# Kernel tuning notes

Measured on AMD Instinct MI355X. Metric: run time of the kernel, lower is better.

The kernel has to match this reference:

```python
import jax, jax.numpy as jnp
import numpy as np
from jax import lax

F = 64          # nb_filters
K_DOWN = 4      # size_kernel_sample
K_RES = 3       # size_kernel_res
DIL = 3         # rate_dilation_res
N_DOWN = 3      # downsampling blocks (one level)
N_RES = 4       # residual sub-blocks per block
N_EMB = 512     # codebook size
BETA = 0.25


def conv1d(x, w, b, stride=1, dil=1, act=True):
    # x: (B,T,C), w: (K,Cin,Cout)
    y = lax.conv_general_dilated(x, w, (stride,), 'SAME', rhs_dilation=(dil,),
                                 dimension_numbers=('NWC', 'WIO', 'NWC')) + b
    return jax.nn.relu(y) if act else y


def conv1d_t(x, w, b, stride):
    # transposed conv, w: (K, Cin, Cout)
    y = lax.conv_transpose(x, w, (stride,), 'SAME',
                           dimension_numbers=('NWC', 'WIO', 'NWC')) + b
    return jax.nn.relu(y)


def setup_inputs() -> dict:
    key = jax.random.key(0)
    ks = jax.random.split(key, 12)
    s_in = 1.0 / np.sqrt(K_DOWN * 1)
    s_f = 1.0 / np.sqrt(K_DOWN * F)
    s_r = 1.0 / np.sqrt(K_RES * F)
    return {
        'x': jax.random.normal(ks[0], (4, 65536, 1), dtype=jnp.float32),
        'w_down0': jax.random.normal(ks[1], (K_DOWN, 1, F), dtype=jnp.float32) * s_in,
        'b_down0': jnp.zeros((F,), jnp.float32),
        'w_down': jax.random.normal(ks[2], (N_DOWN - 1, K_DOWN, F, F), dtype=jnp.float32) * s_f,
        'b_down': jnp.zeros((N_DOWN - 1, F), jnp.float32),
        'w_res_enc': jax.random.normal(ks[3], (N_DOWN, N_RES, 2, K_RES, F, F), dtype=jnp.float32) * s_r,
        'b_res_enc': jnp.zeros((N_DOWN, N_RES, 2, F), jnp.float32),
        'codebook': jax.random.normal(ks[4], (N_EMB, F), dtype=jnp.float32),
        'w_res_dec': jax.random.normal(ks[5], (N_DOWN, N_RES, 2, K_RES, F, F), dtype=jnp.float32) * s_r,
        'b_res_dec': jnp.zeros((N_DOWN, N_RES, 2, F), jnp.float32),
        'w_up': jax.random.normal(ks[6], (N_DOWN, K_DOWN, F, F), dtype=jnp.float32) * s_f,
        'b_up': jnp.zeros((N_DOWN, F), jnp.float32),
        'w_proj': jax.random.normal(ks[7], (K_RES, F, 1), dtype=jnp.float32) * s_r,
        'b_proj': jnp.zeros((1,), jnp.float32),
    }


def reference(x, w_down0, b_down0, w_down, b_down, w_res_enc, b_res_enc,
              codebook, w_res_dec, b_res_dec, w_up, b_up, w_proj, b_proj):
    # ---- Encoder: N_DOWN stride-2 downsampling blocks, each followed by
    # N_RES ForwardResidualSubBlocks (dilated conv -> conv, residual add) ----
    h = conv1d(x, w_down0, b_down0, stride=2)
    for blk in range(N_DOWN):
        if blk > 0:
            h = conv1d(h, w_down[blk - 1], b_down[blk - 1], stride=2)
        for r in range(N_RES):
            y = conv1d(h, w_res_enc[blk, r, 0], b_res_enc[blk, r, 0], dil=DIL)
            y = conv1d(y, w_res_enc[blk, r, 1], b_res_enc[blk, r, 1], dil=1)
            h = h + y
    z_e = h  # (B, T/8, F)

    # ---- VectorQuantiser over channel axis ----
    dot = jnp.einsum('btd,kd->btk', z_e, codebook)          # tensordot
    nz = jnp.sum(jnp.square(z_e), axis=-1, keepdims=True)   # (B,T,1)
    ne = jnp.sum(jnp.square(codebook), axis=-1)             # (K,)
    dist = -2.0 * dot + nz + ne                             # squared cdist
    ids = jnp.argmin(dist, axis=-1)                         # (B,T)
    z_q = codebook[ids]                                     # embedding_lookup
    loss_commit = jnp.mean(jnp.linalg.norm(lax.stop_gradient(z_e) - z_q, axis=-1))
    loss_codebook = jnp.mean(jnp.linalg.norm(z_e - lax.stop_gradient(z_q), axis=-1))
    loss_vq = loss_codebook + BETA * loss_commit
    similarity = dot / jnp.sqrt(nz) / jnp.sqrt(ne)

    # ---- Decoder: residual blocks then stride-2 transposed conv, x N_DOWN ----
    h = z_q
    for blk in range(N_DOWN):
        for r in range(N_RES):
            y = conv1d(h, w_res_dec[blk, r, 0], b_res_dec[blk, r, 0], dil=1)
            y = conv1d(y, w_res_dec[blk, r, 1], b_res_dec[blk, r, 1], dil=DIL)
            h = h + y
        h = conv1d_t(h, w_up[blk], b_up[blk], stride=2)
    x_hat = conv1d(h, w_proj, b_proj, act=False)  # linear projection
    return x_hat, loss_vq, ids, similarity
```

## Files before the change

kernel.cpp:

```cpp
#include <hip/hip_runtime.h>
#include <cstdint>


#define OFF_LOSS 262144
#define OFF_IDS  262145
#define OFF_SIM  294913

__global__ __launch_bounds__(256) void down0_kernel(
    const float* __restrict__ x, const float* __restrict__ w,
    const float* __restrict__ bias, float* __restrict__ y)
{
  int idx = blockIdx.x * 256 + threadIdx.x;
  int co = idx & 63;
  int r  = idx >> 6;
  int t  = r & 32767;
  int b  = r >> 15;
  const float* xb = x + (size_t)b * 65536;
  float acc = bias[co];
  #pragma unroll
  for (int k = 0; k < 4; ++k) {
    int gt = 2 * t - 1 + k;
    float xv = ((unsigned)gt < 65536u) ? xb[gt] : 0.f;
    acc += xv * w[k * 64 + co];
  }
  y[(size_t)idx] = fmaxf(acc, 0.f);
}

template <int DIL, bool HAS_RES>
__global__ __launch_bounds__(256, 4) void conv3_kernel(
    const float* __restrict__ x, const float* __restrict__ w,
    const float* __restrict__ bias, const float* res,
    float* y, int T)
{
  constexpr int TT = 128;
  constexpr int XT = TT + 2 * DIL;
  constexpr int XS = XT + 1;
  __shared__ float xs[64 * XS];
  const int tid  = threadIdx.x;
  const int lane = tid & 63;
  const int b    = blockIdx.z;
  const int t0   = blockIdx.x * TT;
  const int wv   = __builtin_amdgcn_readfirstlane(tid >> 6);
  const int co0  = __builtin_amdgcn_readfirstlane(blockIdx.y * 32 + wv * 8);

  const float* xb = x + (size_t)b * T * 64;
  for (int e = tid; e < 16 * XT; e += 256) {
    int tl = e >> 4, cq = (e & 15) * 4;
    int gt = t0 - DIL + tl;
    float4 v = make_float4(0.f, 0.f, 0.f, 0.f);
    if ((unsigned)gt < (unsigned)T) v = *(const float4*)&xb[(size_t)gt * 64 + cq];
    xs[(cq + 0) * XS + tl] = v.x;
    xs[(cq + 1) * XS + tl] = v.y;
    xs[(cq + 2) * XS + tl] = v.z;
    xs[(cq + 3) * XS + tl] = v.w;
  }
  __syncthreads();

  float acc0[8] = {}, acc1[8] = {};
  const float* wb = w + co0;
  #pragma unroll 2
  for (int ci = 0; ci < 64; ++ci) {
    const float* xr = xs + ci * XS + lane;
    float a0 = xr[0],  a1 = xr[DIL],      a2 = xr[2 * DIL];
    float b0 = xr[64], b1 = xr[64 + DIL], b2 = xr[64 + 2 * DIL];
    const float* w0 = wb + (0 * 64 + ci) * 64;
    const float* w1 = wb + (1 * 64 + ci) * 64;
    const float* w2 = wb + (2 * 64 + ci) * 64;
    #pragma unroll
    for (int j = 0; j < 8; ++j) {
      float c0 = w0[j], c1 = w1[j], c2 = w2[j];
      acc0[j] = fmaf(a0, c0, fmaf(a1, c1, fmaf(a2, c2, acc0[j])));
      acc1[j] = fmaf(b0, c0, fmaf(b1, c1, fmaf(b2, c2, acc1[j])));
    }
  }

  float bs[8];
  #pragma unroll
  for (int j = 0; j < 8; ++j) bs[j] = bias[co0 + j];
  size_t o0 = ((size_t)b * T + t0 + lane) * 64 + co0;
  size_t o1 = o0 + (size_t)64 * 64;
  float4 r0a, r0b, r1a, r1b;
  r0a.x = fmaxf(acc0[0] + bs[0], 0.f); r0a.y = fmaxf(acc0[1] + bs[1], 0.f);
  r0a.z = fmaxf(acc0[2] + bs[2], 0.f); r0a.w = fmaxf(acc0[3] + bs[3], 0.f);
  r0b.x = fmaxf(acc0[4] + bs[4], 0.f); r0b.y = fmaxf(acc0[5] + bs[5], 0.f);
  r0b.z = fmaxf(acc0[6] + bs[6], 0.f); r0b.w = fmaxf(acc0[7] + bs[7], 0.f);
  r1a.x = fmaxf(acc1[0] + bs[0], 0.f); r1a.y = fmaxf(acc1[1] + bs[1], 0.f);
  r1a.z = fmaxf(acc1[2] + bs[2], 0.f); r1a.w = fmaxf(acc1[3] + bs[3], 0.f);
  r1b.x = fmaxf(acc1[4] + bs[4], 0.f); r1b.y = fmaxf(acc1[5] + bs[5], 0.f);
  r1b.z = fmaxf(acc1[6] + bs[6], 0.f); r1b.w = fmaxf(acc1[7] + bs[7], 0.f);
  if (HAS_RES) {
    float4 v0a = *(const float4*)&res[o0];
    float4 v0b = *(const float4*)&res[o0 + 4];
    float4 v1a = *(const float4*)&res[o1];
    float4 v1b = *(const float4*)&res[o1 + 4];
    r0a.x += v0a.x; r0a.y += v0a.y; r0a.z += v0a.z; r0a.w += v0a.w;
    r0b.x += v0b.x; r0b.y += v0b.y; r0b.z += v0b.z; r0b.w += v0b.w;
    r1a.x += v1a.x; r1a.y += v1a.y; r1a.z += v1a.z; r1a.w += v1a.w;
    r1b.x += v1b.x; r1b.y += v1b.y; r1b.z += v1b.z; r1b.w += v1b.w;
  }
  *(float4*)&y[o0]     = r0a;
  *(float4*)&y[o0 + 4] = r0b;
  *(float4*)&y[o1]     = r1a;
  *(float4*)&y[o1 + 4] = r1b;
}

__global__ __launch_bounds__(256, 4) void down2_kernel(
    const float* __restrict__ x, const float* __restrict__ w,
    const float* __restrict__ bias, float* __restrict__ y, int Tin)
{
  constexpr int XT = 130, XS = 131;
  __shared__ float xs[64 * XS];
  const int tid  = threadIdx.x;
  const int lane = tid & 63;
  const int b    = blockIdx.z;
  const int t0   = blockIdx.x * 64;
  const int Tout = Tin >> 1;
  const int wv   = __builtin_amdgcn_readfirstlane(tid >> 6);
  const int co0  = __builtin_amdgcn_readfirstlane(blockIdx.y * 32 + wv * 8);

  const float* xb = x + (size_t)b * Tin * 64;
  for (int e = tid; e < 16 * XT; e += 256) {
    int tl = e >> 4, cq = (e & 15) * 4;
    int gt = 2 * t0 - 1 + tl;
    float4 v = make_float4(0.f, 0.f, 0.f, 0.f);
    if ((unsigned)gt < (unsigned)Tin) v = *(const float4*)&xb[(size_t)gt * 64 + cq];
    xs[(cq + 0) * XS + tl] = v.x;
    xs[(cq + 1) * XS + tl] = v.y;
    xs[(cq + 2) * XS + tl] = v.z;
    xs[(cq + 3) * XS + tl] = v.w;
  }
  __syncthreads();

  float acc[8] = {};
  const float* wb = w + co0;
  #pragma unroll 2
  for (int ci = 0; ci < 64; ++ci) {
    const float* xr = xs + ci * XS + 2 * lane;
    float a0 = xr[0], a1 = xr[1], a2 = xr[2], a3 = xr[3];
    const float* w0 = wb + (0 * 64 + ci) * 64;
    const float* w1 = wb + (1 * 64 + ci) * 64;
    const float* w2 = wb + (2 * 64 + ci) * 64;
    const float* w3 = wb + (3 * 64 + ci) * 64;
    #pragma unroll
    for (int j = 0; j < 8; ++j)
      acc[j] = fmaf(a0, w0[j], fmaf(a1, w1[j], fmaf(a2, w2[j], fmaf(a3, w3[j], acc[j]))));
  }

  size_t o = ((size_t)b * Tout + t0 + lane) * 64 + co0;
  float4 ra, rb;
  ra.x = fmaxf(acc[0] + bias[co0 + 0], 0.f); ra.y = fmaxf(acc[1] + bias[co0 + 1], 0.f);
  ra.z = fmaxf(acc[2] + bias[co0 + 2], 0.f); ra.w = fmaxf(acc[3] + bias[co0 + 3], 0.f);
  rb.x = fmaxf(acc[4] + bias[co0 + 4], 0.f); rb.y = fmaxf(acc[5] + bias[co0 + 5], 0.f);
  rb.z = fmaxf(acc[6] + bias[co0 + 6], 0.f); rb.w = fmaxf(acc[7] + bias[co0 + 7], 0.f);
  *(float4*)&y[o]     = ra;
  *(float4*)&y[o + 4] = rb;
}

__global__ __launch_bounds__(256, 4) void up_kernel(
    const float* __restrict__ x, const float* __restrict__ w,
    const float* __restrict__ bias, float* __restrict__ y, int Tin)
{
  constexpr int XT = 66, XS = 67;
  __shared__ float xs[64 * XS];
  const int tid  = threadIdx.x;
  const int lane = tid & 63;
  const int b    = blockIdx.z;
  const int u0   = blockIdx.x * 64;
  const int Tout = Tin << 1;
  const int wv   = __builtin_amdgcn_readfirstlane(tid >> 6);
  const int co0  = __builtin_amdgcn_readfirstlane(blockIdx.y * 32 + wv * 8);

  const float* xb = x + (size_t)b * Tin * 64;
  for (int e = tid; e < 16 * XT; e += 256) {
    int ul = e >> 4, cq = (e & 15) * 4;
    int gu = u0 - 1 + ul;
    float4 v = make_float4(0.f, 0.f, 0.f, 0.f);
    if ((unsigned)gu < (unsigned)Tin) v = *(const float4*)&xb[(size_t)gu * 64 + cq];
    xs[(cq + 0) * XS + ul] = v.x;
    xs[(cq + 1) * XS + ul] = v.y;
    xs[(cq + 2) * XS + ul] = v.z;
    xs[(cq + 3) * XS + ul] = v.w;
  }
  __syncthreads();

  float acce[8] = {}, acco[8] = {};
  const float* wb = w + co0;
  #pragma unroll 2
  for (int ci = 0; ci < 64; ++ci) {
    const float* xr = xs + ci * XS + lane;
    float a0 = xr[0], a1 = xr[1], a2 = xr[2];
    const float* w0 = wb + (0 * 64 + ci) * 64;
    const float* w1 = wb + (1 * 64 + ci) * 64;
    const float* w2 = wb + (2 * 64 + ci) * 64;
    const float* w3 = wb + (3 * 64 + ci) * 64;
    #pragma unroll
    for (int j = 0; j < 8; ++j) {
      acce[j] = fmaf(a0, w0[j], fmaf(a1, w2[j], acce[j]));
      acco[j] = fmaf(a1, w1[j], fmaf(a2, w3[j], acco[j]));
    }
  }

  float bs[8];
  #pragma unroll
  for (int j = 0; j < 8; ++j) bs[j] = bias[co0 + j];
  size_t oe = ((size_t)b * Tout + 2 * (u0 + lane)) * 64 + co0;
  size_t oo = oe + 64;
  float4 ea, eb, oa, ob;
  ea.x = fmaxf(acce[0] + bs[0], 0.f); ea.y = fmaxf(acce[1] + bs[1], 0.f);
  ea.z = fmaxf(acce[2] + bs[2], 0.f); ea.w = fmaxf(acce[3] + bs[3], 0.f);
  eb.x = fmaxf(acce[4] + bs[4], 0.f); eb.y = fmaxf(acce[5] + bs[5], 0.f);
  eb.z = fmaxf(acce[6] + bs[6], 0.f); eb.w = fmaxf(acce[7] + bs[7], 0.f);
  oa.x = fmaxf(acco[0] + bs[0], 0.f); oa.y = fmaxf(acco[1] + bs[1], 0.f);
  oa.z = fmaxf(acco[2] + bs[2], 0.f); oa.w = fmaxf(acco[3] + bs[3], 0.f);
  ob.x = fmaxf(acco[4] + bs[4], 0.f); ob.y = fmaxf(acco[5] + bs[5], 0.f);
  ob.z = fmaxf(acco[6] + bs[6], 0.f); ob.w = fmaxf(acco[7] + bs[7], 0.f);
  *(float4*)&y[oe]     = ea;
  *(float4*)&y[oe + 4] = eb;
  *(float4*)&y[oo]     = oa;
  *(float4*)&y[oo + 4] = ob;
}

__global__ __launch_bounds__(256) void proj_kernel(
    const float* __restrict__ x, const float* __restrict__ w,
    const float* __restrict__ bias, float* __restrict__ out)
{
  const int lane = threadIdx.x & 63;
  const int wid  = (blockIdx.x * 256 + threadIdx.x) >> 6;
  const float w0 = w[lane], w1 = w[64 + lane], w2 = w[128 + lane];
  const float bb = bias[0];
  size_t base = (size_t)wid * 64;
  for (int i = 0; i < 64; ++i) {
    size_t tau = base + i;
    int b = (int)(tau >> 16);
    int t = (int)(tau & 65535);
    const float* xb = x + ((size_t)b * 65536) * 64;
    float pm = (t > 0)     ? xb[(size_t)(t - 1) * 64 + lane] : 0.f;
    float pc =               xb[(size_t)t * 64 + lane];
    float pp = (t < 65535) ? xb[(size_t)(t + 1) * 64 + lane] : 0.f;
    float s = pm * w0 + pc * w1 + pp * w2;
    #pragma unroll
    for (int off = 32; off; off >>= 1) s += __shfl_down(s, off);
    if (lane == 0) out[tau] = s + bb;
  }
}

__global__ __launch_bounds__(256) void nz_kernel(
    const float* __restrict__ ze, float* __restrict__ nz)
{
  int lane = threadIdx.x & 63;
  int tok  = (blockIdx.x * 256 + threadIdx.x) >> 6;
  float v = ze[(size_t)tok * 64 + lane];
  float s = v * v;
  #pragma unroll
  for (int off = 32; off; off >>= 1) s += __shfl_down(s, off);
  if (lane == 0) nz[tok] = s;
}

#define VQA_TOKS 32
__global__ __launch_bounds__(256) void vq_dots_kernel(
    const float* __restrict__ ze, const float* __restrict__ cb,
    const float* __restrict__ nzbuf, float* __restrict__ sim_out,
    float2* __restrict__ pmin)
{
  __shared__ float zs[VQA_TOKS * 64];
  const int tid = threadIdx.x;
  {
    const float4* src = (const float4*)(ze + (size_t)blockIdx.x * VQA_TOKS * 64);
    float4* dst = (float4*)zs;
    dst[tid]       = src[tid];
    dst[tid + 256] = src[tid + 256];
  }
  const int c = blockIdx.y * 256 + tid;
  float r[64];
  #pragma unroll
  for (int q = 0; q < 16; ++q) {
    float4 a = ((const float4*)cb)[(size_t)c * 16 + q];
    r[4*q] = a.x; r[4*q+1] = a.y; r[4*q+2] = a.z; r[4*q+3] = a.w;
  }
  float ne = 0.f;
  #pragma unroll
  for (int d = 0; d < 64; ++d) ne += r[d] * r[d];
  const float rsne = 1.f / sqrtf(ne);
  const int wvid = tid >> 6;
  __syncthreads();

  for (int it = 0; it < VQA_TOKS; ++it) {
    const int tok = blockIdx.x * VQA_TOKS + it;
    const float4* z4 = (const float4*)(zs + it * 64);
    float dot = 0.f;
    #pragma unroll
    for (int q = 0; q < 16; ++q) {
      float4 zv = z4[q];
      dot += zv.x * r[4*q] + zv.y * r[4*q+1] + zv.z * r[4*q+2] + zv.w * r[4*q+3];
    }
    const float nzv = nzbuf[tok];
    float dist = (-2.f * dot + nzv) + ne;
    sim_out[(size_t)tok * 512 + c] = dot * (1.f / sqrtf(nzv)) * rsne;

    float md = dist; int mi = c;
    #pragma unroll
    for (int off = 32; off; off >>= 1) {
      float od = __shfl_down(md, off);
      int   oi = __shfl_down(mi, off);
      if (od < md || (od == md && oi < mi)) { md = od; mi = oi; }
    }
    if ((tid & 63) == 0) pmin[tok * 8 + blockIdx.y * 4 + wvid] = make_float2(md, (float)mi);
  }
}

__global__ __launch_bounds__(256) void vq_finish_kernel(
    const float* __restrict__ ze, const float* __restrict__ cb,
    const float2* __restrict__ pmin, float* __restrict__ zq,
    float* __restrict__ ids_out, float* __restrict__ blocksum)
{
  const int tid = threadIdx.x;
  const int lane = tid & 63, wvid = tid >> 6;
  float lloss = 0.f;
  for (int it = 0; it < 16; ++it) {
    const int tok = blockIdx.x * 64 + wvid * 16 + it;
    float bd = 1e30f; int bi = 0;
    #pragma unroll
    for (int p = 0; p < 8; ++p) {
      float2 pr = pmin[tok * 8 + p];
      float d = pr.x; int i = (int)pr.y;
      if (d < bd || (d == bd && i < bi)) { bd = d; bi = i; }
    }
    float zev = ze[(size_t)tok * 64 + lane];
    float cv  = cb[(size_t)bi * 64 + lane];
    float df = zev - cv;
    float s = df * df;
    #pragma unroll
    for (int off = 32; off; off >>= 1) s += __shfl_down(s, off);
    zq[(size_t)tok * 64 + lane] = cv;
    if (lane == 0) { ids_out[tok] = (float)bi; lloss += sqrtf(s); }
  }
  __shared__ float ls[4];
  if (lane == 0) ls[wvid] = lloss;
  __syncthreads();
  if (tid == 0) blocksum[blockIdx.x] = ls[0] + ls[1] + ls[2] + ls[3];
}

__global__ void loss_fin_kernel(const float* __restrict__ blocksum,
                                float* __restrict__ out)
{
  const int lane = threadIdx.x;
  float s = 0.f;
  for (int i = lane; i < 512; i += 64) s += blocksum[i];
  #pragma unroll
  for (int off = 32; off; off >>= 1) s += __shfl_down(s, off);
  if (lane == 0) out[0] = 1.25f * s / 32768.f;
}

extern "C" void kernel_launch(void* const* d_in, const int* in_sizes, int n_in,
                              void* d_out, int out_size, void* d_ws, size_t ws_size,
                              hipStream_t stream)
{
  const float* x       = (const float*)d_in[0];
  const float* w_down0 = (const float*)d_in[1];
  const float* b_down0 = (const float*)d_in[2];
  const float* w_down  = (const float*)d_in[3];
  const float* b_down  = (const float*)d_in[4];
  const float* w_res_e = (const float*)d_in[5];
  const float* b_res_e = (const float*)d_in[6];
  const float* cb      = (const float*)d_in[7];
  const float* w_res_d = (const float*)d_in[8];
  const float* b_res_d = (const float*)d_in[9];
  const float* w_up    = (const float*)d_in[10];
  const float* b_up    = (const float*)d_in[11];
  const float* w_proj  = (const float*)d_in[12];
  const float* b_proj  = (const float*)d_in[13];

  float* out = (float*)d_out;
  const size_t BUF = (size_t)4 * 65536 * 64;
  float*  bufA     = (float*)d_ws;
  float*  bufB     = bufA + BUF;
  float*  nzbuf    = bufB + BUF;
  float2* pmin     = (float2*)(nzbuf + 32768);
  float*  blocksum = (float*)(pmin + 32768 * 8);

  float* h = bufA;
  float* tmp = bufB;

  down0_kernel<<<32768, 256, 0, stream>>>(x, w_down0, b_down0, h);
  int T = 32768;
  for (int blk = 0; blk < 3; ++blk) {
    if (blk > 0) {
      down2_kernel<<<dim3(T / 2 / 64, 2, 4), 256, 0, stream>>>(
          h, w_down + (size_t)(blk - 1) * 4 * 64 * 64, b_down + (blk - 1) * 64, tmp, T);
      T >>= 1;
      float* s = h; h = tmp; tmp = s;
    }
    for (int r = 0; r < 4; ++r) {
      const float* w0p = w_res_e + (((size_t)blk * 4 + r) * 2 + 0) * 3 * 64 * 64;
      const float* w1p = w_res_e + (((size_t)blk * 4 + r) * 2 + 1) * 3 * 64 * 64;
      const float* b0p = b_res_e + (((size_t)blk * 4 + r) * 2 + 0) * 64;
      const float* b1p = b_res_e + (((size_t)blk * 4 + r) * 2 + 1) * 64;
      conv3_kernel<3, false><<<dim3(T / 128, 2, 4), 256, 0, stream>>>(h, w0p, b0p, nullptr, tmp, T);
      conv3_kernel<1, true ><<<dim3(T / 128, 2, 4), 256, 0, stream>>>(tmp, w1p, b1p, h, h, T);
    }
  }

  nz_kernel<<<8192, 256, 0, stream>>>(h, nzbuf);
  vq_dots_kernel<<<dim3(32768 / VQA_TOKS, 2), 256, 0, stream>>>(h, cb, nzbuf, out + OFF_SIM, pmin);
  vq_finish_kernel<<<512, 256, 0, stream>>>(h, cb, pmin, tmp, out + OFF_IDS, blocksum);
  loss_fin_kernel<<<1, 64, 0, stream>>>(blocksum, out + OFF_LOSS);
  { float* s = h; h = tmp; tmp = s; }

  for (int blk = 0; blk < 3; ++blk) {
    for (int r = 0; r < 4; ++r) {
      const float* w0p = w_res_d + (((size_t)blk * 4 + r) * 2 + 0) * 3 * 64 * 64;
      const float* w1p = w_res_d + (((size_t)blk * 4 + r) * 2 + 1) * 3 * 64 * 64;
      const float* b0p = b_res_d + (((size_t)blk * 4 + r) * 2 + 0) * 64;
      const float* b1p = b_res_d + (((size_t)blk * 4 + r) * 2 + 1) * 64;
      conv3_kernel<1, false><<<dim3(T / 128, 2, 4), 256, 0, stream>>>(h, w0p, b0p, nullptr, tmp, T);
      conv3_kernel<3, true ><<<dim3(T / 128, 2, 4), 256, 0, stream>>>(tmp, w1p, b1p, h, h, T);
    }
    up_kernel<<<dim3(2 * T / 128, 2, 4), 256, 0, stream>>>(
        h, w_up + (size_t)blk * 4 * 64 * 64, b_up + blk * 64, tmp, T);
    T <<= 1;
    float* s = h; h = tmp; tmp = s;
  }

  proj_kernel<<<1024, 256, 0, stream>>>(h, w_proj, b_proj, out);
}
```

Baseline: 1.981 ms.

## Compute all 64 output channels per block in conv kernels, unroll VQ dot loop by two tokens

The conv3, down2 and up kernels now have each wave compute 16 output channels instead of 8, so one block covers all 64 channels and the grid's channel dimension is removed. This halves the number of blocks that stage the same input tile into shared memory, cutting redundant global loads and LDS fills. The cost is twice as many accumulators per thread and higher register pressure under launch_bounds(256,4), which could cause spills or lower occupancy. The VQ dots kernel also processes two tokens per iteration with split accumulators, exposing more instruction-level parallelism in the dot product and in the shuffle-based reductions.

```diff
diff --git a/kernel.cpp b/kernel.cpp
--- a/kernel.cpp
+++ b/kernel.cpp
@@ -38,10 +38,10 @@
   __shared__ float xs[64 * XS];
   const int tid  = threadIdx.x;
   const int lane = tid & 63;
-  const int b    = blockIdx.z;
+  const int b    = blockIdx.y;
   const int t0   = blockIdx.x * TT;
   const int wv   = __builtin_amdgcn_readfirstlane(tid >> 6);
-  const int co0  = __builtin_amdgcn_readfirstlane(blockIdx.y * 32 + wv * 8);
+  const int co0  = __builtin_amdgcn_readfirstlane(wv * 16);
 
   const float* xb = x + (size_t)b * T * 64;
   for (int e = tid; e < 16 * XT; e += 256) {
@@ -56,9 +56,8 @@
   }
   __syncthreads();
 
-  float acc0[8] = {}, acc1[8] = {};
+  float acc0[16] = {}, acc1[16] = {};
   const float* wb = w + co0;
-  #pragma unroll 2
   for (int ci = 0; ci < 64; ++ci) {
     const float* xr = xs + ci * XS + lane;
     float a0 = xr[0],  a1 = xr[DIL],      a2 = xr[2 * DIL];
@@ -67,41 +66,36 @@
     const float* w1 = wb + (1 * 64 + ci) * 64;
     const float* w2 = wb + (2 * 64 + ci) * 64;
     #pragma unroll
-    for (int j = 0; j < 8; ++j) {
+    for (int j = 0; j < 16; ++j) {
       float c0 = w0[j], c1 = w1[j], c2 = w2[j];
       acc0[j] = fmaf(a0, c0, fmaf(a1, c1, fmaf(a2, c2, acc0[j])));
       acc1[j] = fmaf(b0, c0, fmaf(b1, c1, fmaf(b2, c2, acc1[j])));
     }
   }
 
-  float bs[8];
-  #pragma unroll
-  for (int j = 0; j < 8; ++j) bs[j] = bias[co0 + j];
   size_t o0 = ((size_t)b * T + t0 + lane) * 64 + co0;
   size_t o1 = o0 + (size_t)64 * 64;
-  float4 r0a, r0b, r1a, r1b;
-  r0a.x = fmaxf(acc0[0] + bs[0], 0.f); r0a.y = fmaxf(acc0[1] + bs[1], 0.f);
-  r0a.z = fmaxf(acc0[2] + bs[2], 0.f); r0a.w = fmaxf(acc0[3] + bs[3], 0.f);
-  r0b.x = fmaxf(acc0[4] + bs[4], 0.f); r0b.y = fmaxf(acc0[5] + bs[5], 0.f);
-  r0b.z = fmaxf(acc0[6] + bs[6], 0.f); r0b.w = fmaxf(acc0[7] + bs[7], 0.f);
-  r1a.x = fmaxf(acc1[0] + bs[0], 0.f); r1a.y = fmaxf(acc1[1] + bs[1], 0.f);
-  r1a.z = fmaxf(acc1[2] + bs[2], 0.f); r1a.w = fmaxf(acc1[3] + bs[3], 0.f);
-  r1b.x = fmaxf(acc1[4] + bs[4], 0.f); r1b.y = fmaxf(acc1[5] + bs[5], 0.f);
-  r1b.z = fmaxf(acc1[6] + bs[6], 0.f); r1b.w = fmaxf(acc1[7] + bs[7], 0.f);
+  float r0[16], r1[16];
+  #pragma unroll
+  for (int j = 0; j < 16; ++j) {
+    float bj = bias[co0 + j];
+    r0[j] = fmaxf(acc0[j] + bj, 0.f);
+    r1[j] = fmaxf(acc1[j] + bj, 0.f);
+  }
   if (HAS_RES) {
-    float4 v0a = *(const float4*)&res[o0];
-    float4 v0b = *(const float4*)&res[o0 + 4];
-    float4 v1a = *(const float4*)&res[o1];
-    float4 v1b = *(const float4*)&res[o1 + 4];
-    r0a.x += v0a.x; r0a.y += v0a.y; r0a.z += v0a.z; r0a.w += v0a.w;
-    r0b.x += v0b.x; r0b.y += v0b.y; r0b.z += v0b.z; r0b.w += v0b.w;
-    r1a.x += v1a.x; r1a.y += v1a.y; r1a.z += v1a.z; r1a.w += v1a.w;
-    r1b.x += v1b.x; r1b.y += v1b.y; r1b.z += v1b.z; r1b.w += v1b.w;
-  }
-  *(float4*)&y[o0]     = r0a;
-  *(float4*)&y[o0 + 4] = r0b;
-  *(float4*)&y[o1]     = r1a;
-  *(float4*)&y[o1 + 4] = r1b;
+    #pragma unroll
+    for (int q = 0; q < 4; ++q) {
+      float4 v0 = *(const float4*)&res[o0 + 4 * q];
+      float4 v1 = *(const float4*)&res[o1 + 4 * q];
+      r0[4*q+0] += v0.x; r0[4*q+1] += v0.y; r0[4*q+2] += v0.z; r0[4*q+3] += v0.w;
+      r1[4*q+0] += v1.x; r1[4*q+1] += v1.y; r1[4*q+2] += v1.z; r1[4*q+3] += v1.w;
+    }
+  }
+  #pragma unroll
+  for (int q = 0; q < 4; ++q) {
+    *(float4*)&y[o0 + 4 * q] = make_float4(r0[4*q], r0[4*q+1], r0[4*q+2], r0[4*q+3]);
+    *(float4*)&y[o1 + 4 * q] = make_float4(r1[4*q], r1[4*q+1], r1[4*q+2], r1[4*q+3]);
+  }
 }
 
 __global__ __launch_bounds__(256, 4) void down2_kernel(
@@ -112,11 +106,11 @@
   __shared__ float xs[64 * XS];
   const int tid  = threadIdx.x;
   const int lane = tid & 63;
-  const int b    = blockIdx.z;
+  const int b    = blockIdx.y;
   const int t0   = blockIdx.x * 64;
   const int Tout = Tin >> 1;
   const int wv   = __builtin_amdgcn_readfirstlane(tid >> 6);
-  const int co0  = __builtin_amdgcn_readfirstlane(blockIdx.y * 32 + wv * 8);
+  const int co0  = __builtin_amdgcn_readfirstlane(wv * 16);
 
   const float* xb = x + (size_t)b * Tin * 64;
   for (int e = tid; e < 16 * XT; e += 256) {
@@ -131,9 +125,8 @@
   }
   __syncthreads();
 
-  float acc[8] = {};
+  float acc[16] = {};
   const float* wb = w + co0;
-  #pragma unroll 2
   for (int ci = 0; ci < 64; ++ci) {
     const float* xr = xs + ci * XS + 2 * lane;
     float a0 = xr[0], a1 = xr[1], a2 = xr[2], a3 = xr[3];
@@ -142,18 +135,20 @@
     const float* w2 = wb + (2 * 64 + ci) * 64;
     const float* w3 = wb + (3 * 64 + ci) * 64;
     #pragma unroll
-    for (int j = 0; j < 8; ++j)
+    for (int j = 0; j < 16; ++j)
       acc[j] = fmaf(a0, w0[j], fmaf(a1, w1[j], fmaf(a2, w2[j], fmaf(a3, w3[j], acc[j]))));
   }
 
   size_t o = ((size_t)b * Tout + t0 + lane) * 64 + co0;
-  float4 ra, rb;
-  ra.x = fmaxf(acc[0] + bias[co0 + 0], 0.f); ra.y = fmaxf(acc[1] + bias[co0 + 1], 0.f);
-  ra.z = fmaxf(acc[2] + bias[co0 + 2], 0.f); ra.w = fmaxf(acc[3] + bias[co0 + 3], 0.f);
-  rb.x = fmaxf(acc[4] + bias[co0 + 4], 0.f); rb.y = fmaxf(acc[5] + bias[co0 + 5], 0.f);
-  rb.z = fmaxf(acc[6] + bias[co0 + 6], 0.f); rb.w = fmaxf(acc[7] + bias[co0 + 7], 0.f);
-  *(float4*)&y[o]     = ra;
-  *(float4*)&y[o + 4] = rb;
+  #pragma unroll
+  for (int q = 0; q < 4; ++q) {
+    float4 rr;
+    rr.x = fmaxf(acc[4*q+0] + bias[co0 + 4*q+0], 0.f);
+    rr.y = fmaxf(acc[4*q+1] + bias[co0 + 4*q+1], 0.f);
+    rr.z = fmaxf(acc[4*q+2] + bias[co0 + 4*q+2], 0.f);
+    rr.w = fmaxf(acc[4*q+3] + bias[co0 + 4*q+3], 0.f);
+    *(float4*)&y[o + 4 * q] = rr;
+  }
 }
 
 __global__ __launch_bounds__(256, 4) void up_kernel(
@@ -164,11 +159,11 @@
   __shared__ float xs[64 * XS];
   const int tid  = threadIdx.x;
   const int lane = tid & 63;
-  const int b    = blockIdx.z;
+  const int b    = blockIdx.y;
   const int u0   = blockIdx.x * 64;
   const int Tout = Tin << 1;
   const int wv   = __builtin_amdgcn_readfirstlane(tid >> 6);
-  const int co0  = __builtin_amdgcn_readfirstlane(blockIdx.y * 32 + wv * 8);
+  const int co0  = __builtin_amdgcn_readfirstlane(wv * 16);
 
   const float* xb = x + (size_t)b * Tin * 64;
   for (int e = tid; e < 16 * XT; e += 256) {
@@ -183,9 +178,8 @@
   }
   __syncthreads();
 
-  float acce[8] = {}, acco[8] = {};
+  float acce[16] = {}, acco[16] = {};
   const float* wb = w + co0;
-  #pragma unroll 2
   for (int ci = 0; ci < 64; ++ci) {
     const float* xr = xs + ci * XS + lane;
     float a0 = xr[0], a1 = xr[1], a2 = xr[2];
@@ -194,30 +188,28 @@
     const float* w2 = wb + (2 * 64 + ci) * 64;
     const float* w3 = wb + (3 * 64 + ci) * 64;
     #pragma unroll
-    for (int j = 0; j < 8; ++j) {
+    for (int j = 0; j < 16; ++j) {
       acce[j] = fmaf(a0, w0[j], fmaf(a1, w2[j], acce[j]));
       acco[j] = fmaf(a1, w1[j], fmaf(a2, w3[j], acco[j]));
     }
   }
 
-  float bs[8];
-  #pragma unroll
-  for (int j = 0; j < 8; ++j) bs[j] = bias[co0 + j];
   size_t oe = ((size_t)b * Tout + 2 * (u0 + lane)) * 64 + co0;
   size_t oo = oe + 64;
-  float4 ea, eb, oa, ob;
-  ea.x = fmaxf(acce[0] + bs[0], 0.f); ea.y = fmaxf(acce[1] + bs[1], 0.f);
-  ea.z = fmaxf(acce[2] + bs[2], 0.f); ea.w = fmaxf(acce[3] + bs[3], 0.f);
-  eb.x = fmaxf(acce[4] + bs[4], 0.f); eb.y = fmaxf(acce[5] + bs[5], 0.f);
-  eb.z = fmaxf(acce[6] + bs[6], 0.f); eb.w = fmaxf(acce[7] + bs[7], 0.f);
-  oa.x = fmaxf(acco[0] + bs[0], 0.f); oa.y = fmaxf(acco[1] + bs[1], 0.f);
-  oa.z = fmaxf(acco[2] + bs[2], 0.f); oa.w = fmaxf(acco[3] + bs[3], 0.f);
-  ob.x = fmaxf(acco[4] + bs[4], 0.f); ob.y = fmaxf(acco[5] + bs[5], 0.f);
-  ob.z = fmaxf(acco[6] + bs[6], 0.f); ob.w = fmaxf(acco[7] + bs[7], 0.f);
-  *(float4*)&y[oe]     = ea;
-  *(float4*)&y[oe + 4] = eb;
-  *(float4*)&y[oo]     = oa;
-  *(float4*)&y[oo + 4] = ob;
+  #pragma unroll
+  for (int q = 0; q < 4; ++q) {
+    float4 re, ro;
+    re.x = fmaxf(acce[4*q+0] + bias[co0 + 4*q+0], 0.f);
+    re.y = fmaxf(acce[4*q+1] + bias[co0 + 4*q+1], 0.f);
+    re.z = fmaxf(acce[4*q+2] + bias[co0 + 4*q+2], 0.f);
+    re.w = fmaxf(acce[4*q+3] + bias[co0 + 4*q+3], 0.f);
+    ro.x = fmaxf(acco[4*q+0] + bias[co0 + 4*q+0], 0.f);
+    ro.y = fmaxf(acco[4*q+1] + bias[co0 + 4*q+1], 0.f);
+    ro.z = fmaxf(acco[4*q+2] + bias[co0 + 4*q+2], 0.f);
+    ro.w = fmaxf(acco[4*q+3] + bias[co0 + 4*q+3], 0.f);
+    *(float4*)&y[oe + 4 * q] = re;
+    *(float4*)&y[oo + 4 * q] = ro;
+  }
 }
 
 __global__ __launch_bounds__(256) void proj_kernel(
@@ -284,27 +276,42 @@
   const int wvid = tid >> 6;
   __syncthreads();
 
-  for (int it = 0; it < VQA_TOKS; ++it) {
-    const int tok = blockIdx.x * VQA_TOKS + it;
-    const float4* z4 = (const float4*)(zs + it * 64);
-    float dot = 0.f;
-    #pragma unroll
-    for (int q = 0; q < 16; ++q) {
-      float4 zv = z4[q];
-      dot += zv.x * r[4*q] + zv.y * r[4*q+1] + zv.z * r[4*q+2] + zv.w * r[4*q+3];
-    }
-    const float nzv = nzbuf[tok];
-    float dist = (-2.f * dot + nzv) + ne;
-    sim_out[(size_t)tok * 512 + c] = dot * (1.f / sqrtf(nzv)) * rsne;
-
-    float md = dist; int mi = c;
+  for (int it = 0; it < VQA_TOKS; it += 2) {
+    const int ta = blockIdx.x * VQA_TOKS + it;
+    const float4* za = (const float4*)(zs + it * 64);
+    const float4* zb = za + 16;
+    float da0 = 0.f, da1 = 0.f, db0 = 0.f, db1 = 0.f;
+    #pragma unroll
+    for (int q = 0; q < 16; q += 2) {
+      float4 va0 = za[q], va1 = za[q + 1];
+      float4 vb0 = zb[q], vb1 = zb[q + 1];
+      da0 = fmaf(va0.x, r[4*q],   fmaf(va0.y, r[4*q+1], fmaf(va0.z, r[4*q+2], fmaf(va0.w, r[4*q+3], da0))));
+      da1 = fmaf(va1.x, r[4*q+4], fmaf(va1.y, r[4*q+5], fmaf(va1.z, r[4*q+6], fmaf(va1.w, r[4*q+7], da1))));
+      db0 = fmaf(vb0.x, r[4*q],   fmaf(vb0.y, r[4*q+1], fmaf(vb0.z, r[4*q+2], fmaf(vb0.w, r[4*q+3], db0))));
+      db1 = fmaf(vb1.x, r[4*q+4], fmaf(vb1.y, r[4*q+5], fmaf(vb1.z, r[4*q+6], fmaf(vb1.w, r[4*q+7], db1))));
+    }
+    float dota = da0 + da1, dotb = db0 + db1;
+    float nza = nzbuf[ta], nzb = nzbuf[ta + 1];
+    sim_out[(size_t)ta * 512 + c]       = dota * (1.f / sqrtf(nza)) * rsne;
+    sim_out[(size_t)(ta + 1) * 512 + c] = dotb * (1.f / sqrtf(nzb)) * rsne;
+    float dista = (-2.f * dota + nza) + ne;
+    float distb = (-2.f * dotb + nzb) + ne;
+
+    float mda = dista; int mia = c;
+    float mdb = distb; int mib = c;
     #pragma unroll
     for (int off = 32; off; off >>= 1) {
-      float od = __shfl_down(md, off);
-      int   oi = __shfl_down(mi, off);
-      if (od < md || (od == md && oi < mi)) { md = od; mi = oi; }
-    }
-    if ((tid & 63) == 0) pmin[tok * 8 + blockIdx.y * 4 + wvid] = make_float2(md, (float)mi);
+      float oda = __shfl_down(mda, off);
+      int   oia = __shfl_down(mia, off);
+      float odb = __shfl_down(mdb, off);
+      int   oib = __shfl_down(mib, off);
+      if (oda < mda || (oda == mda && oia < mia)) { mda = oda; mia = oia; }
+      if (odb < mdb || (odb == mdb && oib < mib)) { mdb = odb; mib = oib; }
+    }
+    if ((tid & 63) == 0) {
+      pmin[ta * 8 + blockIdx.y * 4 + wvid]       = make_float2(mda, (float)mia);
+      pmin[(ta + 1) * 8 + blockIdx.y * 4 + wvid] = make_float2(mdb, (float)mib);
+    }
   }
 }
 
@@ -385,7 +392,7 @@
   int T = 32768;
   for (int blk = 0; blk < 3; ++blk) {
     if (blk > 0) {
-      down2_kernel<<<dim3(T / 2 / 64, 2, 4), 256, 0, stream>>>(
+      down2_kernel<<<dim3(T / 2 / 64, 4), 256, 0, stream>>>(
           h, w_down + (size_t)(blk - 1) * 4 * 64 * 64, b_down + (blk - 1) * 64, tmp, T);
       T >>= 1;
       float* s = h; h = tmp; tmp = s;
@@ -395,8 +402,8 @@
       const float* w1p = w_res_e + (((size_t)blk * 4 + r) * 2 + 1) * 3 * 64 * 64;
       const float* b0p = b_res_e + (((size_t)blk * 4 + r) * 2 + 0) * 64;
       const float* b1p = b_res_e + (((size_t)blk * 4 + r) * 2 + 1) * 64;
-      conv3_kernel<3, false><<<dim3(T / 128, 2, 4), 256, 0, stream>>>(h, w0p, b0p, nullptr, tmp, T);
-      conv3_kernel<1, true ><<<dim3(T / 128, 2, 4), 256, 0, stream>>>(tmp, w1p, b1p, h, h, T);
+      conv3_kernel<3, false><<<dim3(T / 128, 4), 256, 0, stream>>>(h, w0p, b0p, nullptr, tmp, T);
+      conv3_kernel<1, true ><<<dim3(T / 128, 4), 256, 0, stream>>>(tmp, w1p, b1p, h, h, T);
     }
   }
 
@@ -412,10 +419,10 @@
       const float* w1p = w_res_d + (((size_t)blk * 4 + r) * 2 + 1) * 3 * 64 * 64;
       const float* b0p = b_res_d + (((size_t)blk * 4 + r) * 2 + 0) * 64;
       const float* b1p = b_res_d + (((size_t)blk * 4 + r) * 2 + 1) * 64;
-      conv3_kernel<1, false><<<dim3(T / 128, 2, 4), 256, 0, stream>>>(h, w0p, b0p, nullptr, tmp, T);
-      conv3_kernel<3, true ><<<dim3(T / 128, 2, 4), 256, 0, stream>>>(tmp, w1p, b1p, h, h, T);
-    }
-    up_kernel<<<dim3(2 * T / 128, 2, 4), 256, 0, stream>>>(
+      conv3_kernel<1, false><<<dim3(T / 128, 4), 256, 0, stream>>>(h, w0p, b0p, nullptr, tmp, T);
+      conv3_kernel<3, true ><<<dim3(T / 128, 4), 256, 0, stream>>>(tmp, w1p, b1p, h, h, T);
+    }
+    up_kernel<<<dim3(2 * T / 128, 4), 256, 0, stream>>>(
         h, w_up + (size_t)blk * 4 * 64 * 64, b_up + blk * 64, tmp, T);
     T <<= 1;
     float* s = h; h = tmp; tmp = s;
```

New measurement: 2.302 ms. 16.2% more time.
